# Kernel optimization log

Measured on AMD Instinct MI355X. Metric: run time of the kernel, lower is better.

Reference implementation:

```python
import jax, jax.numpy as jnp
import numpy as np
from jax import lax

# dims
BATCH, SEQ, DMODEL = 2, 2048, 1024
EXPAND, HEADDIM, DSTATE, DCONV, MLP_INNER = 2, 64, 64, 4, 4096
DIN = EXPAND * DMODEL            # 2048
NH = DIN // HEADDIM              # 32 heads
CONV_DIM = DIN + 2 * DSTATE      # x, B, C go through the depthwise conv
DPROJ = 2 * DIN + 2 * DSTATE + NH  # z, xBC, dt
EPS = 1e-5


def rmsnorm(x, w):
    return x * lax.rsqrt(jnp.mean(x * x, axis=-1, keepdims=True) + EPS) * w


def setup_inputs() -> dict:
    key = jax.random.key(0)
    ks = jax.random.split(key, 12)
    n = lambda i, shape, scale: jax.random.normal(ks[i], shape, jnp.float32) * scale
    return {
        "hidden_tokens": n(0, (BATCH, SEQ, DMODEL), 1.0),
        "W_in": n(1, (DMODEL, DPROJ), DMODEL ** -0.5),
        "conv_w": n(2, (CONV_DIM, DCONV), 0.2),
        "conv_b": jnp.zeros((CONV_DIM,), jnp.float32),
        "dt_bias": jax.random.uniform(ks[3], (NH,), jnp.float32, -4.0, -1.0),
        "A_log": jnp.log(jax.random.uniform(ks[4], (NH,), jnp.float32, 1.0, 16.0)),
        "D_param": n(5, (NH,), 1.0),
        "norm_w": jnp.ones((DIN,), jnp.float32),
        "W_out": n(6, (DIN, DMODEL), DIN ** -0.5),
        "rms_w": jnp.ones((DMODEL,), jnp.float32),
        "mlp_w1": n(7, (DMODEL, MLP_INNER), DMODEL ** -0.5),
        "mlp_b1": jnp.zeros((MLP_INNER,), jnp.float32),
        "mlp_w2": n(8, (MLP_INNER, DMODEL), MLP_INNER ** -0.5),
        "mlp_b2": jnp.zeros((DMODEL,), jnp.float32),
    }


def _mamba2(x, W_in, conv_w, conv_b, dt_bias, A_log, D_param, norm_w, W_out):
    b, l, _ = x.shape
    zxbcdt = x @ W_in                                   # (b,l,DPROJ)
    z = zxbcdt[..., :DIN]
    xBC = zxbcdt[..., DIN:DIN + CONV_DIM]
    dt = zxbcdt[..., DIN + CONV_DIM:]                   # (b,l,NH)

    # depthwise causal conv1d over sequence
    xt = jnp.pad(xBC, ((0, 0), (DCONV - 1, 0), (0, 0))).transpose(0, 2, 1)  # (b,c,l+pad)
    conv = lax.conv_general_dilated(xt, conv_w[:, None, :], (1,), "VALID",
                                    feature_group_count=CONV_DIM,
                                    dimension_numbers=("NCH", "OIH", "NCH"))
    xBC = jax.nn.silu(conv.transpose(0, 2, 1) + conv_b)  # (b,l,CONV_DIM)

    xs = xBC[..., :DIN].reshape(b, l, NH, HEADDIM)       # (b,l,h,p)
    Bc = xBC[..., DIN:DIN + DSTATE]                      # (b,l,n), ngroups=1
    Cc = xBC[..., DIN + DSTATE:]                         # (b,l,n)

    dt = jax.nn.softplus(dt + dt_bias)                   # (b,l,h)
    A = -jnp.exp(A_log)                                  # (h,)
    dA = jnp.exp(dt * A)                                 # (b,l,h)
    dtx = dt[..., None] * xs                             # (b,l,h,p)

    def step(h, inp):
        dA_t, dtx_t, B_t, C_t = inp                      # (b,h),(b,h,p),(b,n),(b,n)
        h = dA_t[..., None, None] * h + dtx_t[..., None] * B_t[:, None, None, :]
        y = jnp.einsum("bhpn,bn->bhp", h, C_t)
        return h, y

    h0 = jnp.zeros((b, NH, HEADDIM, DSTATE), x.dtype)
    _, ys = lax.scan(step, h0, (dA.transpose(1, 0, 2), dtx.transpose(1, 0, 2, 3),
                                Bc.transpose(1, 0, 2), Cc.transpose(1, 0, 2)))
    y = ys.transpose(1, 0, 2, 3) + D_param[None, None, :, None] * xs  # (b,l,h,p)
    y = y.reshape(b, l, DIN)
    y = rmsnorm(y * jax.nn.silu(z), norm_w)              # gated RMSNorm
    return y @ W_out


def reference(hidden_tokens, W_in, conv_w, conv_b, dt_bias, A_log, D_param,
              norm_w, W_out, rms_w, mlp_w1, mlp_b1, mlp_w2, mlp_b2):
    h = hidden_tokens + _mamba2(hidden_tokens, W_in, conv_w, conv_b, dt_bias,
                                A_log, D_param, norm_w, W_out)
    hn = rmsnorm(h, rms_w)
    mlp = jax.nn.silu(hn @ mlp_w1 + mlp_b1) @ mlp_w2 + mlp_b2
    return h + mlp
```

## Files before the change

kernel.cpp:

```cpp
#include <hip/hip_runtime.h>
#include <hip/hip_bf16.h>
#include <cstdint>
#include <cstddef>

#define BATCH 2
#define SEQ 2048
#define DMODEL 1024
#define DIN 2048
#define NH 32
#define HEADDIM 64
#define DSTATE 64
#define DCONV 4
#define CONV_DIM (DIN + 2 * DSTATE)
#define DPROJ (2 * DIN + 2 * DSTATE + NH)
#define MLP_INNER 4096
#define TOKENS (BATCH * SEQ)
#define EPS 1e-5f
#define Q 64
#define NCHUNK (SEQ / Q)
#define NCH (BATCH * NCHUNK * NH)
#define LSTR 72
#define BSTR 68
#define NPAD_IN 4352

typedef __attribute__((ext_vector_type(8))) short short8;
typedef __attribute__((ext_vector_type(8))) __bf16 bf16x8;
typedef __attribute__((ext_vector_type(4))) float f32x4;

__device__ inline short f2bf(float f) {
    unsigned u = __builtin_bit_cast(unsigned, f);
    u = (u + 0x7FFFu + ((u >> 16) & 1u)) >> 16;
    return (short)u;
}
__device__ inline float bf2f(short s) {
    unsigned u = ((unsigned)(unsigned short)s) << 16;
    return __builtin_bit_cast(float, u);
}
__device__ inline float silu_f(float x) { return x / (1.f + __expf(-x)); }

__device__ inline bf16x8 ld_frag(const short* p) {
    short8 s = *(const short8*)p;
    return __builtin_bit_cast(bf16x8, s);
}

__device__ inline void glds16(const short* g, short* l) {
    __builtin_amdgcn_global_load_lds(
        (const __attribute__((address_space(1))) void*)g,
        (__attribute__((address_space(3))) void*)l, 16, 0, 0);
}

template <int MODE>
__global__ __launch_bounds__(512, 4) void gemm_bf16_kernel(
    const short* __restrict__ A, const short* __restrict__ BT,
    void* __restrict__ Cout, const float* __restrict__ bias,
    int M, int N, int K)
{
    constexpr int KT = 64;
    const int tid  = threadIdx.x;
    const int wid  = tid >> 6;
    const int lane = tid & 63;
    const int lm   = lane & 15;
    const int lg   = lane >> 4;
    const int wm   = (wid >> 2) * 64;
    const int wn   = (wid & 3) * 32;

    const int nb  = gridDim.x * gridDim.y;
    const int bid = blockIdx.y * gridDim.x + blockIdx.x;
    const int per = nb >> 3;
    const int nid = (bid & 7) * per + (bid >> 3);
    const int m0  = (nid / gridDim.x) * 128;
    const int n0  = (nid % gridDim.x) * 128;

    __shared__ __attribute__((aligned(16))) short Al0[128 * KT];
    __shared__ __attribute__((aligned(16))) short Al1[128 * KT];
    __shared__ __attribute__((aligned(16))) short Bl0[128 * KT];
    __shared__ __attribute__((aligned(16))) short Bl1[128 * KT];

    f32x4 acc[4][2];
#pragma unroll
    for (int i = 0; i < 4; ++i)
#pragma unroll
        for (int j = 0; j < 2; ++j) acc[i][j] = {0.f, 0.f, 0.f, 0.f};

    const int srow = lane >> 3;
    const int scb  = (lane & 7) ^ srow;
    const short* Ag = A  + (size_t)(m0 + wid * 16 + srow) * K + scb * 8;
    const short* Bg = BT + (size_t)(n0 + wid * 16 + srow) * K + scb * 8;
    const int woff = wid * 16 * KT;

    const int niter = K / KT;
    {
#pragma unroll
        for (int j = 0; j < 2; ++j) {
            glds16(Ag + (size_t)j * 8 * K, Al0 + woff + j * 512);
            glds16(Bg + (size_t)j * 8 * K, Bl0 + woff + j * 512);
        }
    }

    for (int i = 0; i < niter; ++i) {
        __syncthreads();
        const short* Ac = (i & 1) ? Al1 : Al0;
        const short* Bc = (i & 1) ? Bl1 : Bl0;
        if (i + 1 < niter) {
            int kt = (i + 1) * KT;
            short* al = ((i & 1) ? Al0 : Al1) + woff;
            short* bl = ((i & 1) ? Bl0 : Bl1) + woff;
#pragma unroll
            for (int j = 0; j < 2; ++j) {
                glds16(Ag + kt + (size_t)j * 8 * K, al + j * 512);
                glds16(Bg + kt + (size_t)j * 8 * K, bl + j * 512);
            }
        }

#pragma unroll
        for (int sub = 0; sub < 2; ++sub) {
            const int cb = sub * 4 + lg;
            bf16x8 af[4], bf[2];
#pragma unroll
            for (int ii = 0; ii < 4; ++ii) {
                int ar = wm + ii * 16 + lm;
                af[ii] = ld_frag(&Ac[ar * KT + ((cb ^ (ar & 7)) * 8)]);
            }
#pragma unroll
            for (int j = 0; j < 2; ++j) {
                int br = wn + j * 16 + lm;
                bf[j] = ld_frag(&Bc[br * KT + ((cb ^ (br & 7)) * 8)]);
            }
#pragma unroll
            for (int ii = 0; ii < 4; ++ii)
#pragma unroll
                for (int j = 0; j < 2; ++j)
                    acc[ii][j] = __builtin_amdgcn_mfma_f32_16x16x32_bf16(af[ii], bf[j], acc[ii][j], 0, 0, 0);
        }
    }

#pragma unroll
    for (int j = 0; j < 2; ++j) {
        int col = n0 + wn + j * 16 + lm;
        if (col >= N) continue;
        float bv = (MODE == 1) ? bias[col] : 0.f;
#pragma unroll
        for (int i = 0; i < 4; ++i) {
#pragma unroll
            for (int r = 0; r < 4; ++r) {
                int row = m0 + wm + i * 16 + lg * 4 + r;
                float v = acc[i][j][r];
                if (MODE == 1) v = silu_f(v + bv);
                ((short*)Cout)[(size_t)row * N + col] = f2bf(v);
            }
        }
    }
}

template <int MODE>
__global__ __launch_bounds__(512, 4) void gemm64_kernel(
    const short* __restrict__ A, const short* __restrict__ BT,
    void* __restrict__ Cout, const float* __restrict__ bias,
    const float* __restrict__ res, int M, int N, int K)
{
    constexpr int KT = 64;
    const int tid  = threadIdx.x;
    const int wid  = tid >> 6;
    const int lane = tid & 63;
    const int lm   = lane & 15;
    const int lg   = lane >> 4;
    const int wm   = (wid >> 2) * 32;
    const int wn   = (wid & 3) * 32;

    const int nb  = gridDim.x * gridDim.y;
    const int bid = blockIdx.y * gridDim.x + blockIdx.x;
    const int per = nb >> 3;
    const int nid = (bid & 7) * per + (bid >> 3);
    const int m0  = (nid / gridDim.x) * 64;
    const int n0  = (nid % gridDim.x) * 128;

    __shared__ __attribute__((aligned(16))) short Al0[64 * KT];
    __shared__ __attribute__((aligned(16))) short Al1[64 * KT];
    __shared__ __attribute__((aligned(16))) short Bl0[128 * KT];
    __shared__ __attribute__((aligned(16))) short Bl1[128 * KT];

    f32x4 acc[2][2];
#pragma unroll
    for (int i = 0; i < 2; ++i)
#pragma unroll
        for (int j = 0; j < 2; ++j) acc[i][j] = {0.f, 0.f, 0.f, 0.f};

    const int srow = lane >> 3;
    const int scb  = (lane & 7) ^ srow;
    const short* Bg = BT + (size_t)(n0 + wid * 16 + srow) * K + scb * 8;
    const short* Ag = A  + (size_t)(m0 + (wid & 3) * 16 + srow) * K + scb * 8;
    const int woffB = wid * 16 * KT;
    const int woffA = (wid & 3) * 16 * KT;
    const bool doA = (wid < 4);

    const int niter = K / KT;
    {
#pragma unroll
        for (int j = 0; j < 2; ++j) {
            if (doA) glds16(Ag + (size_t)j * 8 * K, Al0 + woffA + j * 512);
            glds16(Bg + (size_t)j * 8 * K, Bl0 + woffB + j * 512);
        }
    }

    for (int i = 0; i < niter; ++i) {
        __syncthreads();
        const short* Ac = (i & 1) ? Al1 : Al0;
        const short* Bc = (i & 1) ? Bl1 : Bl0;
        if (i + 1 < niter) {
            int kt = (i + 1) * KT;
            short* al = ((i & 1) ? Al0 : Al1) + woffA;
            short* bl = ((i & 1) ? Bl0 : Bl1) + woffB;
#pragma unroll
            for (int j = 0; j < 2; ++j) {
                if (doA) glds16(Ag + kt + (size_t)j * 8 * K, al + j * 512);
                glds16(Bg + kt + (size_t)j * 8 * K, bl + j * 512);
            }
        }

#pragma unroll
        for (int sub = 0; sub < 2; ++sub) {
            const int cb = sub * 4 + lg;
            bf16x8 af[2], bf[2];
#pragma unroll
            for (int ii = 0; ii < 2; ++ii) {
                int ar = wm + ii * 16 + lm;
                af[ii] = ld_frag(&Ac[ar * KT + ((cb ^ (ar & 7)) * 8)]);
            }
#pragma unroll
            for (int j = 0; j < 2; ++j) {
                int br = wn + j * 16 + lm;
                bf[j] = ld_frag(&Bc[br * KT + ((cb ^ (br & 7)) * 8)]);
            }
#pragma unroll
            for (int ii = 0; ii < 2; ++ii)
#pragma unroll
                for (int j = 0; j < 2; ++j)
                    acc[ii][j] = __builtin_amdgcn_mfma_f32_16x16x32_bf16(af[ii], bf[j], acc[ii][j], 0, 0, 0);
        }
    }

#pragma unroll
    for (int j = 0; j < 2; ++j) {
        int col = n0 + wn + j * 16 + lm;
        float bv = (MODE == 2) ? bias[col] : 0.f;
#pragma unroll
        for (int i = 0; i < 2; ++i) {
#pragma unroll
            for (int r = 0; r < 4; ++r) {
                int row = m0 + wm + i * 16 + lg * 4 + r;
                float v = acc[i][j][r] + bv + res[(size_t)row * N + col];
                ((float*)Cout)[(size_t)row * N + col] = v;
            }
        }
    }
}

#define PREP_CVT 4096
#define PREP_T1  (PREP_CVT + 4352)
#define PREP_T2  (PREP_T1 + 2048)
#define PREP_T3  (PREP_T2 + 4096)
#define PREP_T4  (PREP_T3 + 4096)
__global__ __launch_bounds__(256) void prep_kernel(
    const float* __restrict__ x, short* __restrict__ xbf,
    const float* __restrict__ W_in, short* __restrict__ WinT,
    const float* __restrict__ W_out, short* __restrict__ WoutT,
    const float* __restrict__ w1, short* __restrict__ w1T,
    const float* __restrict__ w2, short* __restrict__ w2T)
{
    int blk = blockIdx.x;
    if (blk < PREP_CVT) {
        int i = blk * 256 + threadIdx.x;
        f32x4 v = *(const f32x4*)(x + (size_t)i * 4);
        short4 o;
        o.x = f2bf(v.x); o.y = f2bf(v.y); o.z = f2bf(v.z); o.w = f2bf(v.w);
        *(short4*)(xbf + (size_t)i * 4) = o;
        return;
    }
    __shared__ float t[32][33];
    const float* src; short* dst; int K, N, bx, by;
    if (blk < PREP_T1)      { int l = blk - PREP_CVT; bx = l % 136; by = l / 136; src = W_in;  dst = WinT;  K = DMODEL;    N = DPROJ; }
    else if (blk < PREP_T2) { int l = blk - PREP_T1;  bx = l % 32;  by = l / 32;  src = W_out; dst = WoutT; K = DIN;       N = DMODEL; }
    else if (blk < PREP_T3) { int l = blk - PREP_T2;  bx = l % 128; by = l / 128; src = w1;    dst = w1T;   K = DMODEL;    N = MLP_INNER; }
    else                    { int l = blk - PREP_T3;  bx = l % 32;  by = l / 32;  src = w2;    dst = w2T;   K = MLP_INNER; N = DMODEL; }

    int col = threadIdx.x & 31, row8 = threadIdx.x >> 5;
    int gn = bx * 32 + col;
#pragma unroll
    for (int r = 0; r < 4; ++r) {
        int gk = by * 32 + row8 + r * 8;
        t[row8 + r * 8][col] = (gn < N) ? src[(size_t)gk * N + gn] : 0.f;
    }
    __syncthreads();
#pragma unroll
    for (int r = 0; r < 4; ++r) {
        int n = bx * 32 + row8 + r * 8;
        dst[(size_t)n * K + by * 32 + col] = f2bf(t[col][row8 + r * 8]);
    }
}

#define CTOK 8
__global__ __launch_bounds__(256) void conv_kernel(
    const short* __restrict__ zx, const float* __restrict__ cw,
    const float* __restrict__ cb, short* __restrict__ xBCc,
    const float* __restrict__ dt_bias, const float* __restrict__ A_log,
    float* __restrict__ dtb, float* __restrict__ ldab)
{
    int c4 = blockIdx.y * 256 + threadIdx.x;
    int m0 = blockIdx.x * CTOK;
    if (c4 >= CONV_DIM / 4) {
        int i0 = (int)threadIdx.x - 32;
#pragma unroll
        for (int k = 0; k < 2; ++k) {
            int i = i0 + k * 224;
            if (i < 256) {
                int hh = i & 31;
                int m = m0 + (i >> 5);
                float v = bf2f(zx[(size_t)m * DPROJ + DIN + CONV_DIM + hh]) + dt_bias[hh];
                float dtv_ = (v > 20.f) ? v : log1pf(__expf(v));
                dtb[(size_t)m0 * NH + i]  = dtv_;
                ldab[(size_t)m0 * NH + i] = -__expf(A_log[hh]) * dtv_;
            }
        }
        return;
    }
    int c  = c4 * 4;
    int l0 = m0 & (SEQ - 1);

    const short* base = zx + (size_t)m0 * DPROJ + DIN + c;
    f32x4 win[CTOK + 3];
#pragma unroll
    for (int j = 0; j < CTOK + 3; ++j) {
        int off = j - 3;
        if (l0 + off >= 0) {
            short4 sv = *(const short4*)(base + (ptrdiff_t)off * DPROJ);
            win[j] = {bf2f(sv.x), bf2f(sv.y), bf2f(sv.z), bf2f(sv.w)};
        } else {
            win[j] = {0.f, 0.f, 0.f, 0.f};
        }
    }
    f32x4 w0 = *(const f32x4*)(cw + (c + 0) * DCONV);
    f32x4 w1 = *(const f32x4*)(cw + (c + 1) * DCONV);
    f32x4 w2 = *(const f32x4*)(cw + (c + 2) * DCONV);
    f32x4 w3 = *(const f32x4*)(cw + (c + 3) * DCONV);
    f32x4 bb = *(const f32x4*)(cb + c);

    short* outp = xBCc + (size_t)m0 * CONV_DIM + c;
#pragma unroll
    for (int t = 0; t < CTOK; ++t) {
        f32x4 a = {bb.x, bb.y, bb.z, bb.w};
#pragma unroll
        for (int j = 0; j < DCONV; ++j) {
            f32x4 v = win[t + j];
            a.x += v.x * w0[j];
            a.y += v.y * w1[j];
            a.z += v.z * w2[j];
            a.w += v.w * w3[j];
        }
        short4 o;
        o.x = f2bf(silu_f(a.x)); o.y = f2bf(silu_f(a.y));
        o.z = f2bf(silu_f(a.z)); o.w = f2bf(silu_f(a.w));
        *(short4*)(outp + (size_t)t * CONV_DIM) = o;
    }
}

__global__ __launch_bounds__(256) void chunk_kernel(
    const short* __restrict__ xBCc, const float* __restrict__ dtb,
    const float* __restrict__ ldab, short* __restrict__ ybuf,
    short* __restrict__ Sbuf, float* __restrict__ cumdecay)
{
    int bid = blockIdx.x;
    int h = bid & 31, c = (bid >> 5) & 31, b = bid >> 10;
    int m0 = b * SEQ + c * Q;
    int tid = threadIdx.x;
    int wid = tid >> 6, lane = tid & 63, lm = lane & 15, lg = lane >> 4;

    __shared__ __attribute__((aligned(16))) short Cc[64 * LSTR];
    __shared__ __attribute__((aligned(16))) short Bb[64 * LSTR];
    __shared__ __attribute__((aligned(16))) short BwT[64 * LSTR];
    __shared__ __attribute__((aligned(16))) short Xt[64 * LSTR];
    __shared__ __attribute__((aligned(16))) short Mm[64 * LSTR];
    __shared__ float Lc[64], dtv[64];

    if (tid < 64) {
        int s = tid;
        size_t ix = (size_t)(m0 + s) * NH + h;
        float ld = ldab[ix];
        float dt = dtb[ix];
        float v = ld;
#pragma unroll
        for (int off = 1; off < 64; off <<= 1) {
            float o = __shfl_up(v, off);
            if (s >= off) v += o;
        }
        Lc[s] = v;
        dtv[s] = dt;
        cumdecay[(size_t)bid * 64 + s] = __expf(v);
    }
    {
        int row = tid >> 2, c0 = (tid & 3) * 16;
        const short* pB = xBCc + (size_t)(m0 + row) * CONV_DIM + DIN;
#pragma unroll
        for (int u = 0; u < 2; ++u) {
            short8 vb = *(const short8*)(pB + c0 + 8 * u);
            short8 vc = *(const short8*)(pB + DSTATE + c0 + 8 * u);
            *(short8*)&Bb[row * LSTR + c0 + 8 * u] = vb;
            *(short8*)&Cc[row * LSTR + c0 + 8 * u] = vc;
        }
    }
    __syncthreads();
    {
        int s = tid >> 2, c0 = (tid & 3) * 16;
        float w = dtv[s];
        float w2 = __expf(Lc[63] - Lc[s]);
        const short* pX = xBCc + (size_t)(m0 + s) * CONV_DIM + h * HEADDIM;
#pragma unroll
        for (int u = 0; u < 4; ++u) {
            short4 v = *(const short4*)(pX + c0 + 4 * u);
            Xt[(c0 + 4 * u + 0) * LSTR + s] = f2bf(bf2f(v.x) * w);
            Xt[(c0 + 4 * u + 1) * LSTR + s] = f2bf(bf2f(v.y) * w);
            Xt[(c0 + 4 * u + 2) * LSTR + s] = f2bf(bf2f(v.z) * w);
            Xt[(c0 + 4 * u + 3) * LSTR + s] = f2bf(bf2f(v.w) * w);
            short4 sb = *(short4*)&Bb[s * LSTR + c0 + 4 * u];
            BwT[(c0 + 4 * u + 0) * LSTR + s] = f2bf(bf2f(sb.x) * w2);
            BwT[(c0 + 4 * u + 1) * LSTR + s] = f2bf(bf2f(sb.y) * w2);
            BwT[(c0 + 4 * u + 2) * LSTR + s] = f2bf(bf2f(sb.z) * w2);
            BwT[(c0 + 4 * u + 3) * LSTR + s] = f2bf(bf2f(sb.w) * w2);
        }
    }
    __syncthreads();

    {
        bf16x8 af[2];
#pragma unroll
        for (int kk = 0; kk < 2; ++kk)
            af[kk] = ld_frag(&Cc[(wid * 16 + lm) * LSTR + kk * 32 + lg * 8]);
#pragma unroll
        for (int j = 0; j < 4; ++j) {
            f32x4 acc = {0.f, 0.f, 0.f, 0.f};
#pragma unroll
            for (int kk = 0; kk < 2; ++kk) {
                bf16x8 bf = ld_frag(&Bb[(j * 16 + lm) * LSTR + kk * 32 + lg * 8]);
                acc = __builtin_amdgcn_mfma_f32_16x16x32_bf16(af[kk], bf, acc, 0, 0, 0);
            }
            int s = j * 16 + lm;
            float Ls = Lc[s];
#pragma unroll
            for (int r = 0; r < 4; ++r) {
                int t = wid * 16 + lg * 4 + r;
                float val = (s <= t) ? acc[r] * __expf(Lc[t] - Ls) : 0.f;
                Mm[t * LSTR + s] = f2bf(val);
            }
        }
    }
    __syncthreads();

    {
        bf16x8 am[2], aw[2];
#pragma unroll
        for (int kk = 0; kk < 2; ++kk) {
            am[kk] = ld_frag(&Mm[(wid * 16 + lm) * LSTR + kk * 32 + lg * 8]);
            aw[kk] = ld_frag(&BwT[(wid * 16 + lm) * LSTR + kk * 32 + lg * 8]);
        }
#pragma unroll
        for (int j = 0; j < 4; ++j) {
            f32x4 a1 = {0.f, 0.f, 0.f, 0.f};
            f32x4 a2 = {0.f, 0.f, 0.f, 0.f};
#pragma unroll
            for (int kk = 0; kk < 2; ++kk) {
                bf16x8 bx = ld_frag(&Xt[(j * 16 + lm) * LSTR + kk * 32 + lg * 8]);
                a1 = __builtin_amdgcn_mfma_f32_16x16x32_bf16(am[kk], bx, a1, 0, 0, 0);
                a2 = __builtin_amdgcn_mfma_f32_16x16x32_bf16(aw[kk], bx, a2, 0, 0, 0);
            }
            int p = j * 16 + lm;
#pragma unroll
            for (int r = 0; r < 4; ++r) {
                int t = wid * 16 + lg * 4 + r;
                Cc[t * LSTR + p] = f2bf(a1[r]);
                Bb[t * LSTR + p] = f2bf(a2[r]);
            }
        }
    }
    __syncthreads();
    {
        int row = tid >> 2, seg = (tid & 3) * 16;
        short8 y0 = *(short8*)&Cc[row * LSTR + seg];
        short8 y1 = *(short8*)&Cc[row * LSTR + seg + 8];
        short* yb = ybuf + (size_t)(m0 + row) * DIN + h * HEADDIM + seg;
        *(short8*)yb = y0;
        *(short8*)(yb + 8) = y1;
        short8 s0 = *(short8*)&Bb[row * LSTR + seg];
        short8 s1 = *(short8*)&Bb[row * LSTR + seg + 8];
        short* sb = Sbuf + (size_t)bid * 4096 + row * 64 + seg;
        *(short8*)sb = s0;
        *(short8*)(sb + 8) = s1;
    }
}

__global__ __launch_bounds__(256) void state_kernel(
    short* __restrict__ SH, const float* __restrict__ cumdecay)
{
    int bh = blockIdx.x >> 2, st = blockIdx.x & 3;
    int b = bh >> 5, h = bh & 31;
    int off = st * 1024 + threadIdx.x * 4;

    f32x4 H = {0.f, 0.f, 0.f, 0.f};
    int cid = b * NCHUNK * NH + h;
    short4 sv = *(const short4*)(SH + (size_t)cid * 4096 + off);
    float cd_next = cumdecay[(size_t)cid * 64 + 63];

    for (int c = 0; c < NCHUNK; ++c) {
        short4 s4 = sv;
        float cd = cd_next;
        size_t base = (size_t)cid * 4096 + off;
        if (c + 1 < NCHUNK) {
            sv = *(const short4*)(SH + base + (size_t)NH * 4096);
            cd_next = cumdecay[(size_t)(cid + NH) * 64 + 63];
        }
        short4 o;
        o.x = f2bf(H.x); o.y = f2bf(H.y); o.z = f2bf(H.z); o.w = f2bf(H.w);
        *(short4*)(SH + base) = o;
        H.x = cd * H.x + bf2f(s4.x);
        H.y = cd * H.y + bf2f(s4.y);
        H.z = cd * H.z + bf2f(s4.z);
        H.w = cd * H.w + bf2f(s4.w);
        cid += NH;
    }
}

__global__ __launch_bounds__(256) void inter_kernel(
    const short* __restrict__ xBCc, const short* __restrict__ Hin,
    const float* __restrict__ cumdecay, short* __restrict__ ybuf)
{
    int bid = blockIdx.x;
    int h = bid & 31, c = (bid >> 5) & 31, b = bid >> 10;
    int m0 = b * SEQ + c * Q;
    int tid = threadIdx.x;
    int wid = tid >> 6, lane = tid & 63, lm = lane & 15, lg = lane >> 4;

    __shared__ __attribute__((aligned(16))) short base_lds[2 * 64 * LSTR];
    short* Cc = base_lds;
    short* HT = base_lds + 64 * LSTR;
    __shared__ float eLc[64];

    if (tid < 64) eLc[tid] = cumdecay[(size_t)bid * 64 + tid];
    {
        int row = tid >> 2, c0 = (tid & 3) * 16;
        const short* pC = xBCc + (size_t)(m0 + row) * CONV_DIM + DIN + DSTATE;
#pragma unroll
        for (int u = 0; u < 2; ++u) {
            short8 vc = *(const short8*)(pC + c0 + 8 * u);
            *(short8*)&Cc[row * LSTR + c0 + 8 * u] = vc;
        }
        const short* pH = Hin + (size_t)bid * 4096 + row * 64;
        short8 h0 = *(const short8*)(pH + c0);
        short8 h1 = *(const short8*)(pH + c0 + 8);
#pragma unroll
        for (int u = 0; u < 8; ++u) {
            HT[(c0 + u) * LSTR + row]     = h0[u];
            HT[(c0 + 8 + u) * LSTR + row] = h1[u];
        }
    }
    __syncthreads();

    bf16x8 af[2];
#pragma unroll
    for (int kk = 0; kk < 2; ++kk)
        af[kk] = ld_frag(&Cc[(wid * 16 + lm) * LSTR + kk * 32 + lg * 8]);
    f32x4 accs[4];
#pragma unroll
    for (int j = 0; j < 4; ++j) {
        f32x4 acc = {0.f, 0.f, 0.f, 0.f};
#pragma unroll
        for (int kk = 0; kk < 2; ++kk) {
            bf16x8 bh_ = ld_frag(&HT[(j * 16 + lm) * LSTR + kk * 32 + lg * 8]);
            acc = __builtin_amdgcn_mfma_f32_16x16x32_bf16(af[kk], bh_, acc, 0, 0, 0);
        }
        accs[j] = acc;
    }
    __syncthreads();
    {
        float* bnc = (float*)base_lds;
#pragma unroll
        for (int j = 0; j < 4; ++j) {
            int p = j * 16 + lm;
#pragma unroll
            for (int r = 0; r < 4; ++r) {
                int t = wid * 16 + lg * 4 + r;
                bnc[t * BSTR + p] = eLc[t] * accs[j][r];
            }
        }
    }
    __syncthreads();
    {
        float* bnc = (float*)base_lds;
        int row = tid >> 2, seg = (tid & 3) * 16;
        f32x4 b0 = *(f32x4*)&bnc[row * BSTR + seg];
        f32x4 b1 = *(f32x4*)&bnc[row * BSTR + seg + 4];
        f32x4 b2 = *(f32x4*)&bnc[row * BSTR + seg + 8];
        f32x4 b3 = *(f32x4*)&bnc[row * BSTR + seg + 12];
        short* yb = ybuf + (size_t)(m0 + row) * DIN + h * HEADDIM + seg;
        short8 y0 = *(short8*)yb;
        short8 y1 = *(short8*)(yb + 8);
        short8 o0, o1;
#pragma unroll
        for (int u = 0; u < 4; ++u) {
            o0[u]     = f2bf(bf2f(y0[u])     + b0[u]);
            o0[u + 4] = f2bf(bf2f(y0[u + 4]) + b1[u]);
            o1[u]     = f2bf(bf2f(y1[u])     + b2[u]);
            o1[u + 4] = f2bf(bf2f(y1[u + 4]) + b3[u]);
        }
        *(short8*)yb = o0;
        *(short8*)(yb + 8) = o1;
    }
}

__global__ __launch_bounds__(256) void norm1_kernel(
    const short* __restrict__ zx, const short* __restrict__ xBCc,
    const float* __restrict__ Dp, const short* __restrict__ y,
    short* __restrict__ ybf, const float* __restrict__ w)
{
    int m = blockIdx.x;
    int t = threadIdx.x;
    int i0 = t * 8;
    const short8 zv = *(const short8*)(zx + (size_t)m * DPROJ + i0);
    const short8 xv = *(const short8*)(xBCc + (size_t)m * CONV_DIM + i0);
    const short8 yv = *(const short8*)(y + (size_t)m * DIN + i0);
    float Dv = Dp[i0 >> 6];

    float vals[8];
    float ss = 0.f;
#pragma unroll
    for (int j = 0; j < 8; ++j) {
        float v = (bf2f(yv[j]) + Dv * bf2f(xv[j])) * silu_f(bf2f(zv[j]));
        vals[j] = v;
        ss += v * v;
    }
#pragma unroll
    for (int o = 32; o >= 1; o >>= 1) ss += __shfl_xor(ss, o);
    __shared__ float wsum[4];
    if ((t & 63) == 0) wsum[t >> 6] = ss;
    __syncthreads();
    float tot = wsum[0] + wsum[1] + wsum[2] + wsum[3];
    float scale = rsqrtf(tot / (float)DIN + EPS);

    f32x4 w0 = *(const f32x4*)(w + i0);
    f32x4 w1 = *(const f32x4*)(w + i0 + 4);
    short8 ov;
#pragma unroll
    for (int j = 0; j < 8; ++j) {
        float wj = (j < 4) ? w0[j] : w1[j - 4];
        ov[j] = f2bf(vals[j] * scale * wj);
    }
    *(short8*)(ybf + (size_t)m * DIN + i0) = ov;
}

__global__ __launch_bounds__(256) void norm2_kernel(
    const float* __restrict__ hb, short* __restrict__ hnbf, const float* __restrict__ w)
{
    int m = blockIdx.x;
    int t = threadIdx.x;
    int i0 = t * 4;
    f32x4 hv = *(const f32x4*)(hb + (size_t)m * DMODEL + i0);
    float ss = hv.x * hv.x + hv.y * hv.y + hv.z * hv.z + hv.w * hv.w;
#pragma unroll
    for (int o = 32; o >= 1; o >>= 1) ss += __shfl_xor(ss, o);
    __shared__ float wsum[4];
    if ((t & 63) == 0) wsum[t >> 6] = ss;
    __syncthreads();
    float tot = wsum[0] + wsum[1] + wsum[2] + wsum[3];
    float scale = rsqrtf(tot / (float)DMODEL + EPS);
    f32x4 wv = *(const f32x4*)(w + i0);
    short4 ov;
    ov.x = f2bf(hv.x * scale * wv.x);
    ov.y = f2bf(hv.y * scale * wv.y);
    ov.z = f2bf(hv.z * scale * wv.z);
    ov.w = f2bf(hv.w * scale * wv.w);
    *(short4*)(hnbf + (size_t)m * DMODEL + i0) = ov;
}

extern "C" void kernel_launch(void* const* d_in, const int* in_sizes, int n_in,
                              void* d_out, int out_size, void* d_ws, size_t ws_size,
                              hipStream_t stream) {
    const float* x       = (const float*)d_in[0];
    const float* W_in    = (const float*)d_in[1];
    const float* conv_w  = (const float*)d_in[2];
    const float* conv_b  = (const float*)d_in[3];
    const float* dt_bias = (const float*)d_in[4];
    const float* A_log   = (const float*)d_in[5];
    const float* D_param = (const float*)d_in[6];
    const float* norm_w  = (const float*)d_in[7];
    const float* W_out   = (const float*)d_in[8];
    const float* rms_w   = (const float*)d_in[9];
    const float* mlp_w1  = (const float*)d_in[10];
    const float* mlp_b1  = (const float*)d_in[11];
    const float* mlp_w2  = (const float*)d_in[12];
    const float* mlp_b2  = (const float*)d_in[13];
    float* out = (float*)d_out;

    float* ws       = (float*)d_ws;
    float* zxf      = ws;
    float* xBCf     = zxf + (size_t)TOKENS * DPROJ;
    float* dtb      = xBCf + (size_t)TOKENS * CONV_DIM;
    float* ldab     = dtb + (size_t)TOKENS * NH;
    float* cumdecay = ldab + (size_t)TOKENS * NH;
    float* ybuf     = cumdecay + (size_t)TOKENS * NH;
    float* SH       = ybuf + (size_t)TOKENS * DIN;
    float* bfarea   = SH + (size_t)NCH * 4096;

    short* zxb   = (short*)zxf;
    short* xBCb  = (short*)xBCf;
    short* xbf   = (short*)ybuf;
    short* midbf = (short*)ybuf;
    short* ybufs = (short*)ybuf;
    short* SHs   = (short*)SH;
    float* hbuf  = SH;
    short* hnbf  = (short*)(SH + (size_t)TOKENS * DMODEL);

    short* ybf   = (short*)bfarea;
    short* WinT  = ybf + (size_t)TOKENS * DIN;
    short* WoutT = WinT + (size_t)NPAD_IN * DMODEL;
    short* w1T   = WoutT + (size_t)DMODEL * DIN;
    short* w2T   = w1T + (size_t)MLP_INNER * DMODEL;

    dim3 blk(256);
    dim3 blk2(512);

    prep_kernel<<<dim3(PREP_T4), blk, 0, stream>>>(
        x, xbf, W_in, WinT, W_out, WoutT, mlp_w1, w1T, mlp_w2, w2T);

    gemm_bf16_kernel<4><<<dim3(NPAD_IN / 128, TOKENS / 128), blk2, 0, stream>>>(
        xbf, WinT, zxb, nullptr, TOKENS, DPROJ, DMODEL);
    conv_kernel<<<dim3(TOKENS / CTOK, (CONV_DIM / 4 + 255) / 256), blk, 0, stream>>>(
        zxb, conv_w, conv_b, xBCb, dt_bias, A_log, dtb, ldab);
    chunk_kernel<<<dim3(NCH), blk, 0, stream>>>(xBCb, dtb, ldab, ybufs, SHs, cumdecay);
    state_kernel<<<dim3(BATCH * NH * 4), blk, 0, stream>>>(SHs, cumdecay);
    inter_kernel<<<dim3(NCH), blk, 0, stream>>>(xBCb, SHs, cumdecay, ybufs);
    norm1_kernel<<<dim3(TOKENS), blk, 0, stream>>>(zxb, xBCb, D_param, ybufs, ybf, norm_w);
    gemm64_kernel<3><<<dim3(DMODEL / 128, TOKENS / 64), blk2, 0, stream>>>(
        ybf, WoutT, hbuf, nullptr, x, TOKENS, DMODEL, DIN);
    norm2_kernel<<<dim3(TOKENS), blk, 0, stream>>>(hbuf, hnbf, rms_w);
    gemm_bf16_kernel<1><<<dim3(MLP_INNER / 128, TOKENS / 128), blk2, 0, stream>>>(
        hnbf, w1T, midbf, mlp_b1, TOKENS, MLP_INNER, DMODEL);
    gemm64_kernel<2><<<dim3(DMODEL / 128, TOKENS / 64), blk2, 0, stream>>>(
        midbf, w2T, out, mlp_b2, hbuf, TOKENS, DMODEL, MLP_INNER);
}
```

Measured before the change: 363.5 us.

## Move W_out/MLP weight transposes from prep kernel into chunk kernel tail blocks

The prep kernel now converts only x and transposes W_in. The bf16 transposes of W_out, mlp_w1 and mlp_w2 run as 10240 extra blocks appended to the chunk_kernel grid, reusing its shared memory. This shortens the critical path before the first GEMM and lets the weight conversion share the GPU with the chunk scan blocks. The cost is a larger chunk kernel grid with branchy blocks that compete for CUs with the scan work.

```diff
diff --git a/kernel.cpp b/kernel.cpp
--- a/kernel.cpp
+++ b/kernel.cpp
@@ -257,15 +257,9 @@
 
 #define PREP_CVT 4096
 #define PREP_T1  (PREP_CVT + 4352)
-#define PREP_T2  (PREP_T1 + 2048)
-#define PREP_T3  (PREP_T2 + 4096)
-#define PREP_T4  (PREP_T3 + 4096)
 __global__ __launch_bounds__(256) void prep_kernel(
     const float* __restrict__ x, short* __restrict__ xbf,
-    const float* __restrict__ W_in, short* __restrict__ WinT,
-    const float* __restrict__ W_out, short* __restrict__ WoutT,
-    const float* __restrict__ w1, short* __restrict__ w1T,
-    const float* __restrict__ w2, short* __restrict__ w2T)
+    const float* __restrict__ W_in, short* __restrict__ WinT)
 {
     int blk = blockIdx.x;
     if (blk < PREP_CVT) {
@@ -277,24 +271,20 @@
         return;
     }
     __shared__ float t[32][33];
-    const float* src; short* dst; int K, N, bx, by;
-    if (blk < PREP_T1)      { int l = blk - PREP_CVT; bx = l % 136; by = l / 136; src = W_in;  dst = WinT;  K = DMODEL;    N = DPROJ; }
-    else if (blk < PREP_T2) { int l = blk - PREP_T1;  bx = l % 32;  by = l / 32;  src = W_out; dst = WoutT; K = DIN;       N = DMODEL; }
-    else if (blk < PREP_T3) { int l = blk - PREP_T2;  bx = l % 128; by = l / 128; src = w1;    dst = w1T;   K = DMODEL;    N = MLP_INNER; }
-    else                    { int l = blk - PREP_T3;  bx = l % 32;  by = l / 32;  src = w2;    dst = w2T;   K = MLP_INNER; N = DMODEL; }
-
+    int l = blk - PREP_CVT;
+    int bx = l % 136, by = l / 136;
     int col = threadIdx.x & 31, row8 = threadIdx.x >> 5;
     int gn = bx * 32 + col;
 #pragma unroll
     for (int r = 0; r < 4; ++r) {
         int gk = by * 32 + row8 + r * 8;
-        t[row8 + r * 8][col] = (gn < N) ? src[(size_t)gk * N + gn] : 0.f;
+        t[row8 + r * 8][col] = (gn < DPROJ) ? W_in[(size_t)gk * DPROJ + gn] : 0.f;
     }
     __syncthreads();
 #pragma unroll
     for (int r = 0; r < 4; ++r) {
         int n = bx * 32 + row8 + r * 8;
-        dst[(size_t)n * K + by * 32 + col] = f2bf(t[col][row8 + r * 8]);
+        WinT[(size_t)n * DMODEL + by * 32 + col] = f2bf(t[col][row8 + r * 8]);
     }
 }
 
@@ -366,13 +356,13 @@
 __global__ __launch_bounds__(256) void chunk_kernel(
     const short* __restrict__ xBCc, const float* __restrict__ dtb,
     const float* __restrict__ ldab, short* __restrict__ ybuf,
-    short* __restrict__ Sbuf, float* __restrict__ cumdecay)
+    short* __restrict__ Sbuf, float* __restrict__ cumdecay,
+    const float* __restrict__ Wo, short* __restrict__ WoT,
+    const float* __restrict__ w1, short* __restrict__ w1T,
+    const float* __restrict__ w2, short* __restrict__ w2T)
 {
     int bid = blockIdx.x;
-    int h = bid & 31, c = (bid >> 5) & 31, b = bid >> 10;
-    int m0 = b * SEQ + c * Q;
     int tid = threadIdx.x;
-    int wid = tid >> 6, lane = tid & 63, lm = lane & 15, lg = lane >> 4;
 
     __shared__ __attribute__((aligned(16))) short Cc[64 * LSTR];
     __shared__ __attribute__((aligned(16))) short Bb[64 * LSTR];
@@ -381,6 +371,33 @@
     __shared__ __attribute__((aligned(16))) short Mm[64 * LSTR];
     __shared__ float Lc[64], dtv[64];
 
+    if (bid >= NCH) {
+        int l = bid - NCH;
+        const float* src; short* dst; int K, N, bx, by;
+        if (l < 2048)      {           bx = l % 32;  by = l / 32;  src = Wo; dst = WoT; K = DIN;       N = DMODEL; }
+        else if (l < 6144) { l -= 2048; bx = l % 128; by = l / 128; src = w1; dst = w1T; K = DMODEL;    N = MLP_INNER; }
+        else               { l -= 6144; bx = l % 32;  by = l / 32;  src = w2; dst = w2T; K = MLP_INNER; N = DMODEL; }
+        float (*t)[33] = (float(*)[33])Cc;
+        int col = tid & 31, row8 = tid >> 5;
+        int gn = bx * 32 + col;
+#pragma unroll
+        for (int r = 0; r < 4; ++r) {
+            int gk = by * 32 + row8 + r * 8;
+            t[row8 + r * 8][col] = (gn < N) ? src[(size_t)gk * N + gn] : 0.f;
+        }
+        __syncthreads();
+#pragma unroll
+        for (int r = 0; r < 4; ++r) {
+            int n = bx * 32 + row8 + r * 8;
+            dst[(size_t)n * K + by * 32 + col] = f2bf(t[col][row8 + r * 8]);
+        }
+        return;
+    }
+
+    int h = bid & 31, c = (bid >> 5) & 31, b = bid >> 10;
+    int m0 = b * SEQ + c * Q;
+    int wid = tid >> 6, lane = tid & 63, lm = lane & 15, lg = lane >> 4;
+
     if (tid < 64) {
         int s = tid;
         size_t ix = (size_t)(m0 + s) * NH + h;
@@ -411,7 +428,7 @@
     {
         int s = tid >> 2, c0 = (tid & 3) * 16;
         float w = dtv[s];
-        float w2 = __expf(Lc[63] - Lc[s]);
+        float w2_ = __expf(Lc[63] - Lc[s]);
         const short* pX = xBCc + (size_t)(m0 + s) * CONV_DIM + h * HEADDIM;
 #pragma unroll
         for (int u = 0; u < 4; ++u) {
@@ -421,10 +438,10 @@
             Xt[(c0 + 4 * u + 2) * LSTR + s] = f2bf(bf2f(v.z) * w);
             Xt[(c0 + 4 * u + 3) * LSTR + s] = f2bf(bf2f(v.w) * w);
             short4 sb = *(short4*)&Bb[s * LSTR + c0 + 4 * u];
-            BwT[(c0 + 4 * u + 0) * LSTR + s] = f2bf(bf2f(sb.x) * w2);
-            BwT[(c0 + 4 * u + 1) * LSTR + s] = f2bf(bf2f(sb.y) * w2);
-            BwT[(c0 + 4 * u + 2) * LSTR + s] = f2bf(bf2f(sb.z) * w2);
-            BwT[(c0 + 4 * u + 3) * LSTR + s] = f2bf(bf2f(sb.w) * w2);
+            BwT[(c0 + 4 * u + 0) * LSTR + s] = f2bf(bf2f(sb.x) * w2_);
+            BwT[(c0 + 4 * u + 1) * LSTR + s] = f2bf(bf2f(sb.y) * w2_);
+            BwT[(c0 + 4 * u + 2) * LSTR + s] = f2bf(bf2f(sb.z) * w2_);
+            BwT[(c0 + 4 * u + 3) * LSTR + s] = f2bf(bf2f(sb.w) * w2_);
         }
     }
     __syncthreads();
@@ -725,14 +742,15 @@
     dim3 blk(256);
     dim3 blk2(512);
 
-    prep_kernel<<<dim3(PREP_T4), blk, 0, stream>>>(
-        x, xbf, W_in, WinT, W_out, WoutT, mlp_w1, w1T, mlp_w2, w2T);
+    prep_kernel<<<dim3(PREP_T1), blk, 0, stream>>>(x, xbf, W_in, WinT);
 
     gemm_bf16_kernel<4><<<dim3(NPAD_IN / 128, TOKENS / 128), blk2, 0, stream>>>(
         xbf, WinT, zxb, nullptr, TOKENS, DPROJ, DMODEL);
     conv_kernel<<<dim3(TOKENS / CTOK, (CONV_DIM / 4 + 255) / 256), blk, 0, stream>>>(
         zxb, conv_w, conv_b, xBCb, dt_bias, A_log, dtb, ldab);
-    chunk_kernel<<<dim3(NCH), blk, 0, stream>>>(xBCb, dtb, ldab, ybufs, SHs, cumdecay);
+    chunk_kernel<<<dim3(NCH + 10240), blk, 0, stream>>>(
+        xBCb, dtb, ldab, ybufs, SHs, cumdecay,
+        W_out, WoutT, mlp_w1, w1T, mlp_w2, w2T);
     state_kernel<<<dim3(BATCH * NH * 4), blk, 0, stream>>>(SHs, cumdecay);
     inter_kernel<<<dim3(NCH), blk, 0, stream>>>(xBCb, SHs, cumdecay, ybufs);
     norm1_kernel<<<dim3(TOKENS), blk, 0, stream>>>(zxb, xBCb, D_param, ybufs, ybf, norm_w);
```

Result: slower. 387.9 us (+6.7%).
